# Performance work log

Measured on AMD Instinct MI355X. Metric: run time of the kernel, lower is better.

## Reference

```python
import jax, jax.numpy as jnp
import numpy as np


def setup_inputs() -> dict:
    key = jax.random.key(0)
    ks = jax.random.split(key, 6)
    B, S, H, F, E = 4, 2048, 1024, 4096, 8
    x = jax.random.normal(ks[0], (B, S, H), dtype=jnp.float32)
    Wr = jax.random.normal(ks[1], (H, E), dtype=jnp.float32) * (1.0 / np.sqrt(H))
    br = jnp.zeros((E,), dtype=jnp.float32)
    W1 = jax.random.normal(ks[2], (E, H, F), dtype=jnp.float32) * (1.0 / np.sqrt(H))
    b1 = jnp.zeros((E, F), dtype=jnp.float32)
    W2 = jax.random.normal(ks[3], (E, F, H), dtype=jnp.float32) * (1.0 / np.sqrt(F))
    b2 = jnp.zeros((E, H), dtype=jnp.float32)
    b_buf = jnp.zeros((E,), dtype=jnp.float32)  # load-balancing bias buffer, zero-init
    return {"x": x, "b_buf": b_buf, "Wr": Wr, "br": br,
            "W1": W1, "b1": b1, "W2": W2, "b2": b2, "k": 2}


def reference(x, b_buf, Wr, br, W1, b1, W2, b2, k):
    # Router
    scores = jnp.einsum('bsh,he->bse', x, Wr) + br          # [B,S,E]
    probs = jax.nn.softmax(scores, axis=-1)
    # load_balancing: expert selection uses biased scores (b_buf pre-update)
    _, expert_id = jax.lax.top_k(probs + b_buf, k)          # [B,S,k] int
    # combine weights use unbiased probs
    p, _ = jax.lax.top_k(probs, k)                          # [B,S,k]
    # Dense-dispatch reference: run every expert MLP on all tokens,
    # then select via one-hot mask (same math as gather/scatter dispatch).
    h1 = jnp.einsum('bsh,ehf->ebsf', x, W1) + b1[:, None, None, :]
    h1 = jax.nn.gelu(h1, approximate=False)                 # torch nn.GELU = exact
    out_e = jnp.einsum('ebsf,efh->ebsh', h1, W2) + b2[:, None, None, :]
    E = W1.shape[0]
    onehot = (expert_id[None, :, :, :] == jnp.arange(E)[:, None, None, None]).astype(x.dtype)  # [E,B,S,k]
    out_k = jnp.einsum('ebsk,ebsh->bskh', onehot, out_e)    # scatter-combine per slot
    w = p / jnp.sum(p, axis=-1, keepdims=True)              # normalize top-k probs
    return jnp.einsum('bsk,bskh->bsh', w, out_k)
```

## Files before the change

kernel.cpp:

```cpp
#include <hip/hip_runtime.h>
#include <stdint.h>

#define NTOK 8192
#define H_ 1024
#define F_ 4096
#define E_ 8
#define VCAP 18432
#define VMBLK 72
#define NCOMP 16384

using f32x4  = __attribute__((ext_vector_type(4))) float;
using short8 = __attribute__((ext_vector_type(8))) short;

typedef __attribute__((address_space(1))) const uint32_t gu32;
typedef __attribute__((address_space(3))) uint32_t lu32;

__device__ __forceinline__ void glds16(const void* g, void* l) {
  __builtin_amdgcn_global_load_lds((gu32*)g, (lu32*)l, 16, 0, 0);
}

__device__ __forceinline__ ushort f2bf(float f) {
  union { float f; uint32_t u; } v; v.f = f;
  uint32_t r = (v.u + 0x7FFFu + ((v.u >> 16) & 1u)) >> 16;
  return (ushort)r;
}

__device__ __forceinline__ float gelu_t(float x) {
  float u = 0.7978845608028654f * (x + 0.044715f * x * x * x);
  float e = exp2f(u * 2.885390081777927f);
  float th = 1.0f - 2.0f / (1.0f + e);
  return 0.5f * x * (1.0f + th);
}

__global__ void k_init(int* cnt, int* cur, int* tok, float* wl, int* v2c) {
  int i = blockIdx.x * 256 + threadIdx.x;
  if (i < E_) { cnt[i] = 0; cur[i] = 0; }
  if (i < VCAP) { tok[i] = -1; wl[i] = 0.f; v2c[i] = -1; }
}

__global__ __launch_bounds__(256) void k_transcvt(const float* __restrict__ W,
                                                  ushort* __restrict__ WT,
                                                  int R, int C) {
  __shared__ float t[64][65];
  int e = blockIdx.z;
  int c0 = blockIdx.x * 64, r0 = blockIdx.y * 64;
  const float* Wp = W + (size_t)e * R * C;
  ushort* Tp = WT + (size_t)e * R * C;
  int tx = threadIdx.x & 15, ty = threadIdx.x >> 4;
#pragma unroll
  for (int i = 0; i < 4; i++) {
    int lr = ty + i * 16;
    const float4 v = *(const float4*)&Wp[(size_t)(r0 + lr) * C + c0 + tx * 4];
    t[lr][tx * 4 + 0] = v.x; t[lr][tx * 4 + 1] = v.y;
    t[lr][tx * 4 + 2] = v.z; t[lr][tx * 4 + 3] = v.w;
  }
  __syncthreads();
#pragma unroll
  for (int i = 0; i < 4; i++) {
    int lc = ty + i * 16;
    ushort4 o;
    o.x = f2bf(t[tx * 4 + 0][lc]);
    o.y = f2bf(t[tx * 4 + 1][lc]);
    o.z = f2bf(t[tx * 4 + 2][lc]);
    o.w = f2bf(t[tx * 4 + 3][lc]);
    *(ushort4*)&Tp[(size_t)(c0 + lc) * R + r0 + tx * 4] = o;
  }
}

__global__ __launch_bounds__(256) void k_router(const float* __restrict__ x,
                                                const float* __restrict__ Wr,
                                                const float* __restrict__ br,
                                                const float* __restrict__ bbuf,
                                                int* cnt, int* te, float* tw) {
  int wid = threadIdx.x >> 6, lane = threadIdx.x & 63;
  int t = blockIdx.x * 4 + wid;
  const float* xp = x + (size_t)t * H_;
  double acc[E_];
#pragma unroll
  for (int e = 0; e < E_; e++) acc[e] = 0.0;
  for (int j = lane; j < H_; j += 64) {
    float xv = xp[j];
    const float4 w0 = *(const float4*)&Wr[j * 8];
    const float4 w1 = *(const float4*)&Wr[j * 8 + 4];
    acc[0] += (double)xv * (double)w0.x;
    acc[1] += (double)xv * (double)w0.y;
    acc[2] += (double)xv * (double)w0.z;
    acc[3] += (double)xv * (double)w0.w;
    acc[4] += (double)xv * (double)w1.x;
    acc[5] += (double)xv * (double)w1.y;
    acc[6] += (double)xv * (double)w1.z;
    acc[7] += (double)xv * (double)w1.w;
  }
#pragma unroll
  for (int e = 0; e < E_; e++)
    for (int s = 32; s > 0; s >>= 1) acc[e] += __shfl_xor(acc[e], s);
  if (lane == 0) {
    double s[E_], m = -1e300;
    for (int e = 0; e < E_; e++) { s[e] = acc[e] + (double)br[e]; if (s[e] > m) m = s[e]; }
    double pe[E_], sum = 0.0;
    for (int e = 0; e < E_; e++) { pe[e] = exp(s[e] - m); sum += pe[e]; }
    double pr[E_], bb[E_];
    for (int e = 0; e < E_; e++) { pr[e] = pe[e] / sum; bb[e] = pr[e] + (double)bbuf[e]; }
    int e0 = 0;
    for (int e = 1; e < E_; e++) if (bb[e] > bb[e0]) e0 = e;
    int e1 = (e0 == 0) ? 1 : 0;
    for (int e = 0; e < E_; e++) if (e != e0 && bb[e] > bb[e1]) e1 = e;
    int a0 = 0;
    for (int e = 1; e < E_; e++) if (pr[e] > pr[a0]) a0 = e;
    int a1 = (a0 == 0) ? 1 : 0;
    for (int e = 0; e < E_; e++) if (e != a0 && pr[e] > pr[a1]) a1 = e;
    double iv = 1.0 / (pr[a0] + pr[a1]);
    te[t * 2] = e0; te[t * 2 + 1] = e1;
    tw[t * 2] = (float)(pr[a0] * iv); tw[t * 2 + 1] = (float)(pr[a1] * iv);
    atomicAdd(&cnt[e0], 1); atomicAdd(&cnt[e1], 1);
  }
}

__global__ void k_offsets(const int* cnt, int* off, int* coff) {
  if (threadIdx.x == 0 && blockIdx.x == 0) {
    int o = 0, c = 0;
    for (int e = 0; e < E_; e++) {
      off[e] = o; coff[e] = c;
      o += ((cnt[e] + 255) >> 8) << 8;
      c += cnt[e];
    }
    off[E_] = o; coff[E_] = c;
  }
}

__global__ void k_build(const int* __restrict__ te, const float* __restrict__ tw,
                        const int* __restrict__ off, const int* __restrict__ coff,
                        int* cur, int* tok, float* wl, int* v2c, int* ctok) {
  int t = blockIdx.x * 256 + threadIdx.x;
  if (t >= NTOK) return;
#pragma unroll
  for (int s = 0; s < 2; s++) {
    int e = te[t * 2 + s];
    int slot = atomicAdd(&cur[e], 1);
    int vp = off[e] + slot;
    int cp = coff[e] + slot;
    tok[vp] = t; wl[vp] = tw[t * 2 + s]; v2c[vp] = cp; ctok[cp] = t;
  }
}

__global__ __launch_bounds__(256) void k_gather(const float* __restrict__ x,
                                                const int* __restrict__ ctok,
                                                ushort* __restrict__ Xg) {
  int row = blockIdx.x;
  int t = ctok[row];
  const float4* src = (const float4*)(x + (size_t)t * H_);
  ushort4* dst = (ushort4*)(Xg + (size_t)row * H_);
  int i = threadIdx.x;
  float4 v = src[i];
  ushort4 o; o.x = f2bf(v.x); o.y = f2bf(v.y); o.z = f2bf(v.z); o.w = f2bf(v.w);
  dst[i] = o;
}

__global__ void k_zero(float* out) {
  size_t i = (size_t)blockIdx.x * 256 + threadIdx.x;
  float4 z; z.x = 0.f; z.y = 0.f; z.z = 0.f; z.w = 0.f;
  ((float4*)out)[i] = z;
}

template <int MODE>
__global__ __launch_bounds__(512) void k_gemm(const ushort* __restrict__ A,
                                              const ushort* __restrict__ BT,
                                              const float* __restrict__ bias,
                                              ushort* __restrict__ h1,
                                              float* __restrict__ Out,
                                              const int* __restrict__ off,
                                              const int* __restrict__ v2c,
                                              const int* __restrict__ tok,
                                              const float* __restrict__ wl,
                                              int K, int N, int NTe) {
  extern __shared__ char lds[];
  int nwg = gridDim.x;
  int cpx = nwg >> 3;
  int bid = blockIdx.x;
  int lid = (bid & 7) * cpx + (bid >> 3);
  int gsz = NTe << 2;
  int g = lid / gsz, r = lid % gsz;
  int ne = r >> 2, m = (g << 2) + (r & 3);
  int row0 = m << 8;
  if (row0 >= off[E_]) return;
  int e = 0;
  while (off[e + 1] <= row0) e++;
  int n0, k0, nk;
  if (MODE == 0) { n0 = ne << 7; k0 = 0; nk = K >> 6; }
  else           { n0 = (ne >> 1) << 7; k0 = (ne & 1) * (K >> 1); nk = K >> 7; }
  const ushort* Bp = BT + (size_t)e * (size_t)N * (size_t)K;

  int tid = threadIdx.x, lane = tid & 63, w = tid >> 6;
  int wr = w >> 1, wc = w & 1;

  f32x4 acc[4][4];
#pragma unroll
  for (int mm = 0; mm < 4; mm++)
#pragma unroll
    for (int nn = 0; nn < 4; nn++) acc[mm][nn] = (f32x4){0.f, 0.f, 0.f, 0.f};

  int ur = lane >> 2;
  int sgs = ((lane >> 2) & 3) ^ ((lane >> 4) & 3);
  int sc = (lane & 3) ^ sgs;
  int vrA = row0 + (w << 5) + ur;
  int cr0 = v2c[vrA];      if (cr0 < 0) cr0 = 0;
  int cr1 = v2c[vrA + 16]; if (cr1 < 0) cr1 = 0;
  const char* aP0 = (const char*)(A + (size_t)cr0 * K) + k0 * 2 + sc * 16;
  const char* aP1 = (const char*)(A + (size_t)cr1 * K) + k0 * 2 + sc * 16;
  const char* bP0 = (const char*)(Bp + (size_t)(n0 + (w << 4) + ur) * K) + k0 * 2 + sc * 16;

  int fr = lane & 15, fq = lane >> 4;
  int sgf = (fr & 3) ^ ((fr >> 2) & 3);
  int kchunk = (fq ^ sgf) << 3;

#define STAGE(tt, kss, bb) do {                                        \
    size_t kb = (size_t)(tt) * 128 + (size_t)(kss) * 64;               \
    char* ab = lds + (bb) * 49152 + (kss) * 16384;                     \
    char* bbp = lds + (bb) * 49152 + 32768 + (kss) * 8192;             \
    glds16(aP0 + kb, ab + (w << 11));                                  \
    glds16(aP1 + kb, ab + (w << 11) + 1024);                           \
    glds16(bP0 + kb, bbp + (w << 10));                                 \
  } while (0)

#define COMPUTE(bb, kss) do {                                          \
    const ushort* LA = (const ushort*)(lds + (bb) * 49152 + (kss) * 16384); \
    const ushort* LB = (const ushort*)(lds + (bb) * 49152 + 32768 + (kss) * 8192); \
    short8 af[4], bfm[4];                                              \
    _Pragma("unroll")                                                  \
    for (int mm = 0; mm < 4; mm++)                                     \
      af[mm] = *(const short8*)&LA[((wr << 6) + mm * 16 + fr) * 32 + kchunk]; \
    _Pragma("unroll")                                                  \
    for (int nn = 0; nn < 4; nn++)                                     \
      bfm[nn] = *(const short8*)&LB[((wc << 6) + nn * 16 + fr) * 32 + kchunk]; \
    __builtin_amdgcn_s_setprio(1);                                     \
    _Pragma("unroll")                                                  \
    for (int mm = 0; mm < 4; mm++)                                     \
      _Pragma("unroll")                                                \
      for (int nn = 0; nn < 4; nn++)                                   \
        acc[mm][nn] = __builtin_amdgcn_mfma_f32_16x16x32_bf16(af[mm], bfm[nn], acc[mm][nn], 0, 0, 0); \
    __builtin_amdgcn_s_setprio(0);                                     \
  } while (0)

  STAGE(0, 0, 0);
  STAGE(0, 1, 0);
  asm volatile("s_waitcnt vmcnt(3)" ::: "memory");
  __builtin_amdgcn_s_barrier();
  __builtin_amdgcn_sched_barrier(0);

  for (int t = 0; t < nk; t++) {
    int bb = t & 1;
    if (t + 1 < nk) STAGE(t + 1, 0, bb ^ 1);
    COMPUTE(bb, 0);
    if (t + 1 < nk) asm volatile("s_waitcnt vmcnt(3)" ::: "memory");
    else            asm volatile("s_waitcnt vmcnt(0)" ::: "memory");
    __builtin_amdgcn_s_barrier();
    __builtin_amdgcn_sched_barrier(0);
    if (t + 1 < nk) {
      STAGE(t + 1, 1, bb ^ 1);
      COMPUTE(bb, 1);
      asm volatile("s_waitcnt vmcnt(3)" ::: "memory");
      __builtin_amdgcn_s_barrier();
      __builtin_amdgcn_sched_barrier(0);
    } else {
      COMPUTE(bb, 1);
    }
  }
#undef STAGE
#undef COMPUTE

  const float* bp = bias + (size_t)e * N;
  int cbase = n0 + (wc << 6);
  if (MODE == 0) {
#pragma unroll
    for (int mm = 0; mm < 4; mm++) {
#pragma unroll
      for (int j = 0; j < 4; j++) {
        int vr = row0 + (wr << 6) + mm * 16 + (fq << 2) + j;
        int cr = v2c[vr];
        if (cr < 0) continue;
        ushort* hp = h1 + (size_t)cr * N + cbase;
#pragma unroll
        for (int nn = 0; nn < 4; nn++) {
          float v = acc[mm][nn][j] + bp[cbase + nn * 16 + fr];
          hp[nn * 16 + fr] = f2bf(gelu_t(v));
        }
      }
    }
  } else {
    bool addb = (k0 == 0);
#pragma unroll
    for (int mm = 0; mm < 4; mm++) {
#pragma unroll
      for (int j = 0; j < 4; j++) {
        int vr = row0 + (wr << 6) + mm * 16 + (fq << 2) + j;
        int t2 = tok[vr];
        if (t2 < 0) continue;
        float wgt = wl[vr];
#pragma unroll
        for (int nn = 0; nn < 4; nn++) {
          int c = cbase + nn * 16 + fr;
          float v = acc[mm][nn][j] + (addb ? bp[c] : 0.f);
          atomicAdd(&Out[(size_t)t2 * (size_t)N + c], wgt * v);
        }
      }
    }
  }
}

extern "C" void kernel_launch(void* const* d_in, const int* in_sizes, int n_in,
                              void* d_out, int out_size, void* d_ws, size_t ws_size,
                              hipStream_t stream) {
  (void)in_sizes; (void)n_in; (void)out_size; (void)ws_size;
  const float* x    = (const float*)d_in[0];
  const float* bbuf = (const float*)d_in[1];
  const float* Wr   = (const float*)d_in[2];
  const float* br   = (const float*)d_in[3];
  const float* W1   = (const float*)d_in[4];
  const float* b1   = (const float*)d_in[5];
  const float* W2   = (const float*)d_in[6];
  const float* b2   = (const float*)d_in[7];
  float* out = (float*)d_out;

  char* ws = (char*)d_ws;
  ushort* W1T = (ushort*)ws;
  ushort* W2T = (ushort*)(ws + 67108864);
  ushort* Xg  = (ushort*)(ws + 134217728);
  ushort* h1  = (ushort*)(ws + 167772160);
  char* meta  = ws + 301989888;
  int*   cnt  = (int*)(meta);
  int*   off  = (int*)(meta + 64);
  int*   coff = (int*)(meta + 128);
  int*   cur  = (int*)(meta + 192);
  int*   te   = (int*)(meta + 256);
  float* tw   = (float*)(meta + 65792);
  int*   tok  = (int*)(meta + 131328);
  float* wl   = (float*)(meta + 205056);
  int*   v2c  = (int*)(meta + 278784);
  int*   ctok = (int*)(meta + 352512);

  hipFuncSetAttribute((const void*)&k_gemm<0>,
                      hipFuncAttributeMaxDynamicSharedMemorySize, 98304);
  hipFuncSetAttribute((const void*)&k_gemm<1>,
                      hipFuncAttributeMaxDynamicSharedMemorySize, 98304);

  k_init<<<VMBLK, 256, 0, stream>>>(cnt, cur, tok, wl, v2c);
  k_transcvt<<<dim3(F_ / 64, H_ / 64, E_), 256, 0, stream>>>(W1, W1T, H_, F_);
  k_transcvt<<<dim3(H_ / 64, F_ / 64, E_), 256, 0, stream>>>(W2, W2T, F_, H_);
  k_router<<<NTOK / 4, 256, 0, stream>>>(x, Wr, br, bbuf, cnt, te, tw);
  k_offsets<<<1, 64, 0, stream>>>(cnt, off, coff);
  k_build<<<NTOK / 256, 256, 0, stream>>>(te, tw, off, coff, cur, tok, wl, v2c, ctok);
  k_gather<<<NCOMP, 256, 0, stream>>>(x, ctok, Xg);
  k_zero<<<(NTOK * H_ / 4) / 256, 256, 0, stream>>>(out);
  k_gemm<0><<<32 * VMBLK, 512, 98304, stream>>>(Xg, W1T, b1, h1, nullptr,
                                                off, v2c, nullptr, nullptr,
                                                H_, F_, 32);
  k_gemm<1><<<16 * VMBLK, 512, 98304, stream>>>(h1, W2T, b2, nullptr, out,
                                                off, v2c, tok, wl,
                                                F_, H_, 16);
}
```

Measured before the change: 1.040 ms.

## Shrink expert GEMM tiles to 128x128 with single-buffered LDS and 256 threads

```diff
diff --git a/kernel.cpp b/kernel.cpp
--- a/kernel.cpp
+++ b/kernel.cpp
@@ -7,6 +7,7 @@
 #define E_ 8
 #define VCAP 18432
 #define VMBLK 72
+#define MT 144
 #define NCOMP 16384
 
 using f32x4  = __attribute__((ext_vector_type(4))) float;
@@ -163,25 +164,27 @@
 }
 
 template <int MODE>
-__global__ __launch_bounds__(512) void k_gemm(const ushort* __restrict__ A,
-                                              const ushort* __restrict__ BT,
-                                              const float* __restrict__ bias,
-                                              ushort* __restrict__ h1,
-                                              float* __restrict__ Out,
-                                              const int* __restrict__ off,
-                                              const int* __restrict__ v2c,
-                                              const int* __restrict__ tok,
-                                              const float* __restrict__ wl,
-                                              int K, int N, int NTe) {
-  extern __shared__ char lds[];
+__global__ __launch_bounds__(256, 3) void k_gemm(const ushort* __restrict__ A,
+                                                 const ushort* __restrict__ BT,
+                                                 const float* __restrict__ bias,
+                                                 ushort* __restrict__ h1,
+                                                 float* __restrict__ Out,
+                                                 const int* __restrict__ off,
+                                                 const int* __restrict__ v2c,
+                                                 const int* __restrict__ tok,
+                                                 const float* __restrict__ wl,
+                                                 int K, int N, int NTe) {
+  __shared__ __align__(16) ushort As[128 * 64];
+  __shared__ __align__(16) ushort Bs[128 * 64];
+
   int nwg = gridDim.x;
   int cpx = nwg >> 3;
   int bid = blockIdx.x;
   int lid = (bid & 7) * cpx + (bid >> 3);
-  int gsz = NTe << 2;
-  int g = lid / gsz, r = lid % gsz;
-  int ne = r >> 2, m = (g << 2) + (r & 3);
-  int row0 = m << 8;
+  int ng = lid / (MT * 4), r = lid % (MT * 4);
+  int m = r >> 2;
+  int ne = (ng << 2) + (r & 3);
+  int row0 = m << 7;
   if (row0 >= off[E_]) return;
   int e = 0;
   while (off[e + 1] <= row0) e++;
@@ -199,77 +202,60 @@
 #pragma unroll
     for (int nn = 0; nn < 4; nn++) acc[mm][nn] = (f32x4){0.f, 0.f, 0.f, 0.f};
 
-  int ur = lane >> 2;
-  int sgs = ((lane >> 2) & 3) ^ ((lane >> 4) & 3);
-  int sc = (lane & 3) ^ sgs;
-  int vrA = row0 + (w << 5) + ur;
-  int cr0 = v2c[vrA];      if (cr0 < 0) cr0 = 0;
-  int cr1 = v2c[vrA + 16]; if (cr1 < 0) cr1 = 0;
-  const char* aP0 = (const char*)(A + (size_t)cr0 * K) + k0 * 2 + sc * 16;
-  const char* aP1 = (const char*)(A + (size_t)cr1 * K) + k0 * 2 + sc * 16;
-  const char* bP0 = (const char*)(Bp + (size_t)(n0 + (w << 4) + ur) * K) + k0 * 2 + sc * 16;
+  int urow = (w << 3) + (lane >> 3);
+  int sc = (lane & 7) ^ (urow & 7);
+  const char *aP0, *aP1, *aP2, *aP3, *bP0, *bP1, *bP2, *bP3;
+  {
+    size_t kb = (size_t)k0 * 2 + (size_t)sc * 16;
+    int c0 = v2c[row0 + 0 * 32 + urow];  if (c0 < 0) c0 = 0;
+    int c1 = v2c[row0 + 1 * 32 + urow];  if (c1 < 0) c1 = 0;
+    int c2 = v2c[row0 + 2 * 32 + urow];  if (c2 < 0) c2 = 0;
+    int c3 = v2c[row0 + 3 * 32 + urow];  if (c3 < 0) c3 = 0;
+    aP0 = (const char*)(A + (size_t)c0 * K) + kb;
+    aP1 = (const char*)(A + (size_t)c1 * K) + kb;
+    aP2 = (const char*)(A + (size_t)c2 * K) + kb;
+    aP3 = (const char*)(A + (size_t)c3 * K) + kb;
+    bP0 = (const char*)(Bp + (size_t)(n0 + 0 * 32 + urow) * K) + kb;
+    bP1 = (const char*)(Bp + (size_t)(n0 + 1 * 32 + urow) * K) + kb;
+    bP2 = (const char*)(Bp + (size_t)(n0 + 2 * 32 + urow) * K) + kb;
+    bP3 = (const char*)(Bp + (size_t)(n0 + 3 * 32 + urow) * K) + kb;
+  }
 
   int fr = lane & 15, fq = lane >> 4;
-  int sgf = (fr & 3) ^ ((fr >> 2) & 3);
-  int kchunk = (fq ^ sgf) << 3;
-
-#define STAGE(tt, kss, bb) do {                                        \
-    size_t kb = (size_t)(tt) * 128 + (size_t)(kss) * 64;               \
-    char* ab = lds + (bb) * 49152 + (kss) * 16384;                     \
-    char* bbp = lds + (bb) * 49152 + 32768 + (kss) * 8192;             \
-    glds16(aP0 + kb, ab + (w << 11));                                  \
-    glds16(aP1 + kb, ab + (w << 11) + 1024);                           \
-    glds16(bP0 + kb, bbp + (w << 10));                                 \
-  } while (0)
-
-#define COMPUTE(bb, kss) do {                                          \
-    const ushort* LA = (const ushort*)(lds + (bb) * 49152 + (kss) * 16384); \
-    const ushort* LB = (const ushort*)(lds + (bb) * 49152 + 32768 + (kss) * 8192); \
-    short8 af[4], bfm[4];                                              \
-    _Pragma("unroll")                                                  \
-    for (int mm = 0; mm < 4; mm++)                                     \
-      af[mm] = *(const short8*)&LA[((wr << 6) + mm * 16 + fr) * 32 + kchunk]; \
-    _Pragma("unroll")                                                  \
-    for (int nn = 0; nn < 4; nn++)                                     \
-      bfm[nn] = *(const short8*)&LB[((wc << 6) + nn * 16 + fr) * 32 + kchunk]; \
-    __builtin_amdgcn_s_setprio(1);                                     \
-    _Pragma("unroll")                                                  \
-    for (int mm = 0; mm < 4; mm++)                                     \
-      _Pragma("unroll")                                                \
-      for (int nn = 0; nn < 4; nn++)                                   \
-        acc[mm][nn] = __builtin_amdgcn_mfma_f32_16x16x32_bf16(af[mm], bfm[nn], acc[mm][nn], 0, 0, 0); \
-    __builtin_amdgcn_s_setprio(0);                                     \
-  } while (0)
-
-  STAGE(0, 0, 0);
-  STAGE(0, 1, 0);
-  asm volatile("s_waitcnt vmcnt(3)" ::: "memory");
-  __builtin_amdgcn_s_barrier();
-  __builtin_amdgcn_sched_barrier(0);
-
-  for (int t = 0; t < nk; t++) {
-    int bb = t & 1;
-    if (t + 1 < nk) STAGE(t + 1, 0, bb ^ 1);
-    COMPUTE(bb, 0);
-    if (t + 1 < nk) asm volatile("s_waitcnt vmcnt(3)" ::: "memory");
-    else            asm volatile("s_waitcnt vmcnt(0)" ::: "memory");
-    __builtin_amdgcn_s_barrier();
-    __builtin_amdgcn_sched_barrier(0);
-    if (t + 1 < nk) {
-      STAGE(t + 1, 1, bb ^ 1);
-      COMPUTE(bb, 1);
-      asm volatile("s_waitcnt vmcnt(3)" ::: "memory");
-      __builtin_amdgcn_s_barrier();
-      __builtin_amdgcn_sched_barrier(0);
-    } else {
-      COMPUTE(bb, 1);
+  int frs = fr & 7;
+
+  for (int kk = 0; kk < nk; ++kk) {
+    size_t kbo = (size_t)kk * 128;
+    if (kk) __syncthreads();
+    glds16(aP0 + kbo, (char*)As + 0 * 4096 + (w << 10));
+    glds16(bP0 + kbo, (char*)Bs + 0 * 4096 + (w << 10));
+    glds16(aP1 + kbo, (char*)As + 1 * 4096 + (w << 10));
+    glds16(bP1 + kbo, (char*)Bs + 1 * 4096 + (w << 10));
+    glds16(aP2 + kbo, (char*)As + 2 * 4096 + (w << 10));
+    glds16(bP2 + kbo, (char*)Bs + 2 * 4096 + (w << 10));
+    glds16(aP3 + kbo, (char*)As + 3 * 4096 + (w << 10));
+    glds16(bP3 + kbo, (char*)Bs + 3 * 4096 + (w << 10));
+    __syncthreads();
+#pragma unroll
+    for (int ks = 0; ks < 2; ++ks) {
+      short8 af[4], bf[4];
+      int kc = (((ks << 2) + fq) ^ frs) << 3;
+#pragma unroll
+      for (int i = 0; i < 4; ++i)
+        af[i] = *(const short8*)&As[((wr << 6) + i * 16 + fr) * 64 + kc];
+#pragma unroll
+      for (int i = 0; i < 4; ++i)
+        bf[i] = *(const short8*)&Bs[((wc << 6) + i * 16 + fr) * 64 + kc];
+#pragma unroll
+      for (int mm = 0; mm < 4; ++mm)
+#pragma unroll
+        for (int nn = 0; nn < 4; ++nn)
+          acc[mm][nn] = __builtin_amdgcn_mfma_f32_16x16x32_bf16(af[mm], bf[nn], acc[mm][nn], 0, 0, 0);
     }
   }
-#undef STAGE
-#undef COMPUTE
 
   const float* bp = bias + (size_t)e * N;
-  int cbase = n0 + (wc << 6);
+  int cb = n0 + (wc << 6);
   if (MODE == 0) {
 #pragma unroll
     for (int mm = 0; mm < 4; mm++) {
@@ -278,10 +264,10 @@
         int vr = row0 + (wr << 6) + mm * 16 + (fq << 2) + j;
         int cr = v2c[vr];
         if (cr < 0) continue;
-        ushort* hp = h1 + (size_t)cr * N + cbase;
+        ushort* hp = h1 + (size_t)cr * N + cb;
 #pragma unroll
         for (int nn = 0; nn < 4; nn++) {
-          float v = acc[mm][nn][j] + bp[cbase + nn * 16 + fr];
+          float v = acc[mm][nn][j] + bp[cb + nn * 16 + fr];
           hp[nn * 16 + fr] = f2bf(gelu_t(v));
         }
       }
@@ -298,7 +284,7 @@
         float wgt = wl[vr];
 #pragma unroll
         for (int nn = 0; nn < 4; nn++) {
-          int c = cbase + nn * 16 + fr;
+          int c = cb + nn * 16 + fr;
           float v = acc[mm][nn][j] + (addb ? bp[c] : 0.f);
           atomicAdd(&Out[(size_t)t2 * (size_t)N + c], wgt * v);
         }
@@ -338,11 +324,6 @@
   int*   v2c  = (int*)(meta + 278784);
   int*   ctok = (int*)(meta + 352512);
 
-  hipFuncSetAttribute((const void*)&k_gemm<0>,
-                      hipFuncAttributeMaxDynamicSharedMemorySize, 98304);
-  hipFuncSetAttribute((const void*)&k_gemm<1>,
-                      hipFuncAttributeMaxDynamicSharedMemorySize, 98304);
-
   k_init<<<VMBLK, 256, 0, stream>>>(cnt, cur, tok, wl, v2c);
   k_transcvt<<<dim3(F_ / 64, H_ / 64, E_), 256, 0, stream>>>(W1, W1T, H_, F_);
   k_transcvt<<<dim3(H_ / 64, F_ / 64, E_), 256, 0, stream>>>(W2, W2T, F_, H_);
@@ -351,10 +332,10 @@
   k_build<<<NTOK / 256, 256, 0, stream>>>(te, tw, off, coff, cur, tok, wl, v2c, ctok);
   k_gather<<<NCOMP, 256, 0, stream>>>(x, ctok, Xg);
   k_zero<<<(NTOK * H_ / 4) / 256, 256, 0, stream>>>(out);
-  k_gemm<0><<<32 * VMBLK, 512, 98304, stream>>>(Xg, W1T, b1, h1, nullptr,
-                                                off, v2c, nullptr, nullptr,
-                                                H_, F_, 32);
-  k_gemm<1><<<16 * VMBLK, 512, 98304, stream>>>(h1, W2T, b2, nullptr, out,
-                                                off, v2c, tok, wl,
-                                                F_, H_, 16);
-}
+  k_gemm<0><<<32 * MT, 256, 0, stream>>>(Xg, W1T, b1, h1, nullptr,
+                                         off, v2c, nullptr, nullptr,
+                                         H_, F_, 32);
+  k_gemm<1><<<16 * MT, 256, 0, stream>>>(h1, W2T, b2, nullptr, out,
+                                         off, v2c, tok, wl,
+                                         F_, H_, 16);
+}
```

After: 892.9 us. 1.16x faster.
